# Kernel tuning notes

Measured on AMD Instinct MI355X. Metric: run time of the kernel, lower is better.

## Reference

```python
import jax, jax.numpy as jnp
import numpy as np

DT = 0.01
DT_SCALE = 1.0

B, D, R = 4096, 1024, 256

def setup_inputs() -> dict:
    key = jax.random.key(0)
    kx, kv, kf, ku, kw = jax.random.split(key, 5)
    x = jax.random.normal(kx, (B, D), dtype=jnp.float32)
    v = jax.random.normal(kv, (B, D), dtype=jnp.float32)
    force = jax.random.normal(kf, (B, D), dtype=jnp.float32)
    # low-rank Christoffel factors; scaled down so the quadratic term stays stable
    U = jax.random.normal(ku, (D, R), dtype=jnp.float32) * (1.0 / np.sqrt(D))
    W = jax.random.normal(kw, (R, D), dtype=jnp.float32) * (1.0 / np.sqrt(R))
    return {"x": x, "v": v, "force": force, "U": U, "W": W, "steps": 8}

def christoffel(v, U, W):
    # Gamma(v, v) = ((v @ U) ** 2) @ W  -- factored quadratic form
    p = v @ U            # [B, R]
    return (p * p) @ W   # [B, D]

def reference(x, v, force, U, W, steps):
    dt = DT * DT_SCALE

    def step(carry, _):
        cx, cv = carry
        acc = force - christoffel(cv, U, W)
        cx = cx + dt * cv
        cv = cv + dt * acc
        return (cx, cv), None

    (cx, cv), _ = jax.lax.scan(step, (x, v), None, length=steps)
    return (cx, cv)
```

## Files before the change

### kernel.cpp

```cpp
#include <hip/hip_runtime.h>


#define BB 4096
#define DD 1024
#define RR 256
#define DT 0.01f

typedef __attribute__((ext_vector_type(8))) short short8;
typedef __attribute__((ext_vector_type(4))) short short4v;
typedef __attribute__((ext_vector_type(4))) float floatx4;

static __device__ inline unsigned short f2bf(float f) {
    union { float f; unsigned int u; } c; c.f = f;
    unsigned int u = c.u;
    u += 0x7fffu + ((u >> 16) & 1u);
    return (unsigned short)(u >> 16);
}

__global__ __launch_bounds__(1024)
void pack_kernel(const float* __restrict__ U, const float* __restrict__ W,
                 short* __restrict__ Up, short* __restrict__ Wp,
                 short* __restrict__ WUp) {
    __shared__ float red[4][256];
    const int b = blockIdx.x;
    const int tid = threadIdx.x;

    if (b < 128) {
        const bool isU = (b < 64);
        const float* M = isU ? U : W;
        short* P = isU ? Up : Wp;
        const int ld = isU ? RR : DD;
        int t = (isU ? b : b - 64) * 1024 + tid;
        int S = t * 4;
        int j0   = S & 7;
        int lane = (S >> 3) & 63;
        int frag = S >> 9;
        int nl = lane & 15, kq = lane >> 4;
        int kt, nt;
        if (isU) { kt = frag >> 4; nt = frag & 15; }
        else     { kt = frag >> 6; nt = frag & 63; }
        int k0 = kt * 32 + kq * 8 + j0;
        int n  = nt * 16 + nl;
        short4v o;
#pragma unroll
        for (int jj = 0; jj < 4; jj++)
            o[jj] = (short)f2bf(M[(long)(k0 + jj) * ld + n]);
        *(short4v*)(P + S) = o;
    } else {
        const int i  = b - 128;
        const int kk = tid >> 8;
        const int j  = tid & 255;
        const float* wr = W + (long)i * DD + kk * 256;
        const float* uc = U + (long)(kk * 256) * RR + j;
        float a0 = 0.f, a1 = 0.f, a2 = 0.f, a3 = 0.f;
#pragma unroll 8
        for (int m = 0; m < 256; m += 4) {
            a0 += wr[m + 0] * uc[(m + 0) * RR];
            a1 += wr[m + 1] * uc[(m + 1) * RR];
            a2 += wr[m + 2] * uc[(m + 2) * RR];
            a3 += wr[m + 3] * uc[(m + 3) * RR];
        }
        red[kk][j] = (a0 + a1) + (a2 + a3);
        __syncthreads();
        if (tid < 256) {
            float acc = red[0][tid] + red[1][tid] + red[2][tid] + red[3][tid];
            int ktw = i >> 5, kqw = (i >> 3) & 3, jjw = i & 7;
            int ntw = tid >> 4, nlw = tid & 15;
            WUp[(((ktw * 16 + ntw) * 64) + kqw * 16 + nlw) * 8 + jjw] =
                (short)f2bf(acc);
        }
    }
}

__global__ __launch_bounds__(1024)
void euler_kernel(const float* __restrict__ x0,
                  const float* __restrict__ v0,
                  const float* __restrict__ force,
                  const short8* __restrict__ Up,
                  const short8* __restrict__ Wp,
                  const short8* __restrict__ WUp,
                  const int* __restrict__ steps_p,
                  float* __restrict__ out) {
    __shared__ __align__(16) short smem[73984];

    const int tid  = threadIdx.x;
    const int wave = tid >> 6;
    const int lane = tid & 63;
    const int nl   = lane & 15;
    const int quad = lane >> 4;
    const int row0 = blockIdx.x * 16;
    const int steps = steps_p[0];

    short (*va)[1032] = (short(*)[1032])smem;
    short (*fa)[1032] = (short(*)[1032])(smem + 16512);
    short (*q1)[264]  = (short(*)[264])(smem + 65536);
    short (*q2)[264]  = (short(*)[264])(smem + 69760);
    short8* wu8 = (short8*)smem;

    const float4* v04 = (const float4*)v0;
    const float4* f44 = (const float4*)force;
#pragma unroll
    for (int i = 0; i < 4; i++) {
        int idx = tid + i * 1024;
        int row = idx >> 8, c4 = idx & 255;
        long g = (long)(row0 + row) * 256 + c4;
        float4 vv = v04[g];
        float4 ff = f44[g];
        short4v sv, sf;
        sv[0] = (short)f2bf(vv.x); sv[1] = (short)f2bf(vv.y);
        sv[2] = (short)f2bf(vv.z); sv[3] = (short)f2bf(vv.w);
        sf[0] = (short)f2bf(ff.x); sf[1] = (short)f2bf(ff.y);
        sf[2] = (short)f2bf(ff.z); sf[3] = (short)f2bf(ff.w);
        *(short4v*)&va[row][c4 * 4] = sv;
        *(short4v*)&fa[row][c4 * 4] = sf;
    }
    __syncthreads();

    floatx4 P  = {0.f, 0.f, 0.f, 0.f};
    floatx4 FU = {0.f, 0.f, 0.f, 0.f};
#pragma unroll 4
    for (int kt = 0; kt < 32; kt++) {
        short8 av = *(const short8*)&va[nl][kt * 32 + quad * 8];
        short8 af = *(const short8*)&fa[nl][kt * 32 + quad * 8];
        short8 bu = Up[(kt * 16 + wave) * 64 + lane];
        P  = __builtin_amdgcn_mfma_f32_16x16x32_bf16(av, bu, P,  0, 0, 0);
        FU = __builtin_amdgcn_mfma_f32_16x16x32_bf16(af, bu, FU, 0, 0, 0);
    }
    __syncthreads();

#pragma unroll
    for (int i = 0; i < 8; i++)
        wu8[tid + i * 1024] = WUp[tid + i * 1024];

    floatx4 A1 = {0.f, 0.f, 0.f, 0.f};
    floatx4 Q2 = {0.f, 0.f, 0.f, 0.f};
    for (int s = 0; s < steps; s++) {
        short (*pw)[264] = (s & 1) ? q2 : q1;
        float wgt = (float)(steps - 1 - s);
#pragma unroll
        for (int r = 0; r < 4; r++) {
            float g = P[r] * P[r];
            A1[r] += g;
            Q2[r] += wgt * g;
            pw[4 * quad + r][16 * wave + nl] = (short)f2bf(g);
        }
        __syncthreads();
        floatx4 acc = {0.f, 0.f, 0.f, 0.f};
#pragma unroll
        for (int kt = 0; kt < 8; kt++) {
            short8 a = *(const short8*)&pw[nl][kt * 32 + quad * 8];
            short8 b = wu8[(kt * 16 + wave) * 64 + lane];
            acc = __builtin_amdgcn_mfma_f32_16x16x32_bf16(a, b, acc, 0, 0, 0);
        }
#pragma unroll
        for (int r = 0; r < 4; r++)
            P[r] += DT * (FU[r] - acc[r]);
    }
    __syncthreads();

#pragma unroll
    for (int r = 0; r < 4; r++) {
        q1[4 * quad + r][16 * wave + nl] = (short)f2bf(A1[r]);
        q2[4 * quad + r][16 * wave + nl] = (short)f2bf(Q2[r]);
    }
    __syncthreads();

    floatx4 y1[4], y2[4];
#pragma unroll
    for (int t = 0; t < 4; t++) {
        y1[t] = (floatx4){0.f, 0.f, 0.f, 0.f};
        y2[t] = (floatx4){0.f, 0.f, 0.f, 0.f};
    }
#pragma unroll 2
    for (int kt = 0; kt < 8; kt++) {
        short8 a1 = *(const short8*)&q1[nl][kt * 32 + quad * 8];
        short8 a2 = *(const short8*)&q2[nl][kt * 32 + quad * 8];
#pragma unroll
        for (int t = 0; t < 4; t++) {
            short8 b = Wp[(kt * 64 + 4 * wave + t) * 64 + lane];
            y1[t] = __builtin_amdgcn_mfma_f32_16x16x32_bf16(a1, b, y1[t], 0, 0, 0);
            y2[t] = __builtin_amdgcn_mfma_f32_16x16x32_bf16(a2, b, y2[t], 0, 0, 0);
        }
    }

    float (*s1)[1024] = (float(*)[1024])smem;
    float (*s2)[1024] = (float(*)[1024])(smem + 32768);
#pragma unroll
    for (int t = 0; t < 4; t++) {
        int col = 64 * wave + 16 * t + nl;
#pragma unroll
        for (int r = 0; r < 4; r++) {
            int row = 4 * quad + r;
            s1[row][col] = -DT * y1[t][r];
            s2[row][col] = -DT * DT * y2[t][r];
        }
    }
    __syncthreads();

    const float sdt  = steps * DT;
    const float tdt2 = 0.5f * (float)(steps * (steps - 1)) * DT * DT;
    const float4* x4 = (const float4*)x0;
    float4* out4 = (float4*)out;
#pragma unroll
    for (int p = 0; p < 4; p++) {
        int idx = tid + p * 1024;
        int row = idx >> 8, c4 = idx & 255;
        long gi = (long)(row0 + row) * 256 + c4;
        float4 vv = v04[gi];
        float4 ff = f44[gi];
        float4 xx = x4[gi];
        float4 t1 = *(const float4*)&s1[row][c4 * 4];
        float4 t2 = *(const float4*)&s2[row][c4 * 4];
        float4 ox, ov;
        ox.x = xx.x + sdt * vv.x + tdt2 * ff.x + t2.x;
        ox.y = xx.y + sdt * vv.y + tdt2 * ff.y + t2.y;
        ox.z = xx.z + sdt * vv.z + tdt2 * ff.z + t2.z;
        ox.w = xx.w + sdt * vv.w + tdt2 * ff.w + t2.w;
        ov.x = vv.x + sdt * ff.x + t1.x;
        ov.y = vv.y + sdt * ff.y + t1.y;
        ov.z = vv.z + sdt * ff.z + t1.z;
        ov.w = vv.w + sdt * ff.w + t1.w;
        out4[gi] = ox;
        out4[(long)BB * 256 + gi] = ov;
    }
}

extern "C" void kernel_launch(void* const* d_in, const int* in_sizes, int n_in,
                              void* d_out, int out_size, void* d_ws, size_t ws_size,
                              hipStream_t stream) {
    const float* x     = (const float*)d_in[0];
    const float* v     = (const float*)d_in[1];
    const float* force = (const float*)d_in[2];
    const float* U     = (const float*)d_in[3];
    const float* W     = (const float*)d_in[4];
    const int*   steps = (const int*)d_in[5];

    short* Up  = (short*)d_ws;
    short* Wp  = Up + 262144;
    short* WUp = Wp + 262144;

    pack_kernel<<<384, 1024, 0, stream>>>(U, W, Up, Wp, WUp);
    euler_kernel<<<256, 1024, 0, stream>>>(x, v, force,
                                           (const short8*)Up, (const short8*)Wp,
                                           (const short8*)WUp,
                                           steps, (float*)d_out);
}
```

Before: 146.3 us.

## Keep WU fragments in registers, precompute epilogue terms, vectorize WU precompute

The pack kernel's W·U product now has each thread accumulate float4 columns over a 64-row K slice and does a 16-way reduction, giving coalesced vector loads of U. The euler kernel loads its per-wave WU fragments straight into registers instead of staging them in shared memory, which removes one barrier and the LDS reads inside the step loop. It also reads x once up front and precomputes the linear part of the outputs into registers, so v, force and x are not re-read from global memory at the end. In exchange, per-thread register pressure rises (8 short8 plus 8 float4), which could cause spills at 1024 threads per block.

```diff
diff --git a/kernel.cpp b/kernel.cpp
--- a/kernel.cpp
+++ b/kernel.cpp
@@ -21,7 +21,7 @@
 void pack_kernel(const float* __restrict__ U, const float* __restrict__ W,
                  short* __restrict__ Up, short* __restrict__ Wp,
                  short* __restrict__ WUp) {
-    __shared__ float red[4][256];
+    __shared__ float4 red[16][64];
     const int b = blockIdx.x;
     const int tid = threadIdx.x;
 
@@ -48,26 +48,36 @@
         *(short4v*)(P + S) = o;
     } else {
         const int i  = b - 128;
-        const int kk = tid >> 8;
-        const int j  = tid & 255;
-        const float* wr = W + (long)i * DD + kk * 256;
-        const float* uc = U + (long)(kk * 256) * RR + j;
-        float a0 = 0.f, a1 = 0.f, a2 = 0.f, a3 = 0.f;
+        const int ks = tid >> 6;
+        const int j4 = tid & 63;
+        const float4* U4 = (const float4*)U;
+        const float*  wr = W + (long)i * DD + ks * 64;
+        float4 acc = {0.f, 0.f, 0.f, 0.f};
 #pragma unroll 8
-        for (int m = 0; m < 256; m += 4) {
-            a0 += wr[m + 0] * uc[(m + 0) * RR];
-            a1 += wr[m + 1] * uc[(m + 1) * RR];
-            a2 += wr[m + 2] * uc[(m + 2) * RR];
-            a3 += wr[m + 3] * uc[(m + 3) * RR];
-        }
-        red[kk][j] = (a0 + a1) + (a2 + a3);
+        for (int m = 0; m < 64; m++) {
+            float w = wr[m];
+            float4 u = U4[(ks * 64 + m) * 64 + j4];
+            acc.x += w * u.x; acc.y += w * u.y;
+            acc.z += w * u.z; acc.w += w * u.w;
+        }
+        red[ks][j4] = acc;
         __syncthreads();
-        if (tid < 256) {
-            float acc = red[0][tid] + red[1][tid] + red[2][tid] + red[3][tid];
+        if (tid < 64) {
+            float4 a = red[0][tid];
+#pragma unroll
+            for (int s = 1; s < 16; s++) {
+                float4 r = red[s][tid];
+                a.x += r.x; a.y += r.y; a.z += r.z; a.w += r.w;
+            }
             int ktw = i >> 5, kqw = (i >> 3) & 3, jjw = i & 7;
-            int ntw = tid >> 4, nlw = tid & 15;
-            WUp[(((ktw * 16 + ntw) * 64) + kqw * 16 + nlw) * 8 + jjw] =
-                (short)f2bf(acc);
+            float av[4] = {a.x, a.y, a.z, a.w};
+#pragma unroll
+            for (int c = 0; c < 4; c++) {
+                int j = 4 * tid + c;
+                int nt = j >> 4, nl = j & 15;
+                WUp[(((ktw * 16 + nt) * 64) + kqw * 16 + nl) * 8 + jjw] =
+                    (short)f2bf(av[c]);
+            }
         }
     }
 }
@@ -81,7 +91,7 @@
                   const short8* __restrict__ WUp,
                   const int* __restrict__ steps_p,
                   float* __restrict__ out) {
-    __shared__ __align__(16) short smem[73984];
+    __shared__ __align__(16) short smem[74240];
 
     const int tid  = threadIdx.x;
     const int wave = tid >> 6;
@@ -90,15 +100,18 @@
     const int quad = lane >> 4;
     const int row0 = blockIdx.x * 16;
     const int steps = steps_p[0];
+    const float sdt  = steps * DT;
+    const float tdt2 = 0.5f * (float)(steps * (steps - 1)) * DT * DT;
 
     short (*va)[1032] = (short(*)[1032])smem;
     short (*fa)[1032] = (short(*)[1032])(smem + 16512);
-    short (*q1)[264]  = (short(*)[264])(smem + 65536);
-    short (*q2)[264]  = (short(*)[264])(smem + 69760);
-    short8* wu8 = (short8*)smem;
+    short (*q1)[264]  = (short(*)[264])(smem + 33024);
+    short (*q2)[264]  = (short(*)[264])(smem + 37248);
 
     const float4* v04 = (const float4*)v0;
     const float4* f44 = (const float4*)force;
+    const float4* x4  = (const float4*)x0;
+    float4 e1[4], e2[4];
 #pragma unroll
     for (int i = 0; i < 4; i++) {
         int idx = tid + i * 1024;
@@ -106,6 +119,7 @@
         long g = (long)(row0 + row) * 256 + c4;
         float4 vv = v04[g];
         float4 ff = f44[g];
+        float4 xx = x4[g];
         short4v sv, sf;
         sv[0] = (short)f2bf(vv.x); sv[1] = (short)f2bf(vv.y);
         sv[2] = (short)f2bf(vv.z); sv[3] = (short)f2bf(vv.w);
@@ -113,7 +127,21 @@
         sf[2] = (short)f2bf(ff.z); sf[3] = (short)f2bf(ff.w);
         *(short4v*)&va[row][c4 * 4] = sv;
         *(short4v*)&fa[row][c4 * 4] = sf;
-    }
+        e1[i].x = xx.x + sdt * vv.x + tdt2 * ff.x;
+        e1[i].y = xx.y + sdt * vv.y + tdt2 * ff.y;
+        e1[i].z = xx.z + sdt * vv.z + tdt2 * ff.z;
+        e1[i].w = xx.w + sdt * vv.w + tdt2 * ff.w;
+        e2[i].x = vv.x + sdt * ff.x;
+        e2[i].y = vv.y + sdt * ff.y;
+        e2[i].z = vv.z + sdt * ff.z;
+        e2[i].w = vv.w + sdt * ff.w;
+    }
+
+    short8 wu[8];
+#pragma unroll
+    for (int kt = 0; kt < 8; kt++)
+        wu[kt] = WUp[(kt * 16 + wave) * 64 + lane];
+
     __syncthreads();
 
     floatx4 P  = {0.f, 0.f, 0.f, 0.f};
@@ -126,11 +154,6 @@
         P  = __builtin_amdgcn_mfma_f32_16x16x32_bf16(av, bu, P,  0, 0, 0);
         FU = __builtin_amdgcn_mfma_f32_16x16x32_bf16(af, bu, FU, 0, 0, 0);
     }
-    __syncthreads();
-
-#pragma unroll
-    for (int i = 0; i < 8; i++)
-        wu8[tid + i * 1024] = WUp[tid + i * 1024];
 
     floatx4 A1 = {0.f, 0.f, 0.f, 0.f};
     floatx4 Q2 = {0.f, 0.f, 0.f, 0.f};
@@ -149,8 +172,7 @@
 #pragma unroll
         for (int kt = 0; kt < 8; kt++) {
             short8 a = *(const short8*)&pw[nl][kt * 32 + quad * 8];
-            short8 b = wu8[(kt * 16 + wave) * 64 + lane];
-            acc = __builtin_amdgcn_mfma_f32_16x16x32_bf16(a, b, acc, 0, 0, 0);
+            acc = __builtin_amdgcn_mfma_f32_16x16x32_bf16(a, wu[kt], acc, 0, 0, 0);
         }
 #pragma unroll
         for (int r = 0; r < 4; r++)
@@ -184,7 +206,7 @@
     }
 
     float (*s1)[1024] = (float(*)[1024])smem;
-    float (*s2)[1024] = (float(*)[1024])(smem + 32768);
+    float (*s2)[1024] = (float(*)[1024])(smem + 41472);
 #pragma unroll
     for (int t = 0; t < 4; t++) {
         int col = 64 * wave + 16 * t + nl;
@@ -197,29 +219,19 @@
     }
     __syncthreads();
 
-    const float sdt  = steps * DT;
-    const float tdt2 = 0.5f * (float)(steps * (steps - 1)) * DT * DT;
-    const float4* x4 = (const float4*)x0;
     float4* out4 = (float4*)out;
 #pragma unroll
     for (int p = 0; p < 4; p++) {
         int idx = tid + p * 1024;
         int row = idx >> 8, c4 = idx & 255;
         long gi = (long)(row0 + row) * 256 + c4;
-        float4 vv = v04[gi];
-        float4 ff = f44[gi];
-        float4 xx = x4[gi];
         float4 t1 = *(const float4*)&s1[row][c4 * 4];
         float4 t2 = *(const float4*)&s2[row][c4 * 4];
         float4 ox, ov;
-        ox.x = xx.x + sdt * vv.x + tdt2 * ff.x + t2.x;
-        ox.y = xx.y + sdt * vv.y + tdt2 * ff.y + t2.y;
-        ox.z = xx.z + sdt * vv.z + tdt2 * ff.z + t2.z;
-        ox.w = xx.w + sdt * vv.w + tdt2 * ff.w + t2.w;
-        ov.x = vv.x + sdt * ff.x + t1.x;
-        ov.y = vv.y + sdt * ff.y + t1.y;
-        ov.z = vv.z + sdt * ff.z + t1.z;
-        ov.w = vv.w + sdt * ff.w + t1.w;
+        ox.x = e1[p].x + t2.x;  ox.y = e1[p].y + t2.y;
+        ox.z = e1[p].z + t2.z;  ox.w = e1[p].w + t2.w;
+        ov.x = e2[p].x + t1.x;  ov.y = e2[p].y + t1.y;
+        ov.z = e2[p].z + t1.z;  ov.w = e2[p].w + t1.w;
         out4[gi] = ox;
         out4[(long)BB * 256 + gi] = ov;
     }
```

Measured after the change: 149.3 us. +2.1%, slower.
